# Kernel optimization log

Hardware: AMD Instinct MI355X
Metric: run time of the kernel (lower is better)

## Reference

```python
import jax, jax.numpy as jnp
import numpy as np

BASE_RES = 16; DESIRED_RES = 8192; LEVEL_INTERVAL = 2
LEVEL_DIM = 4; LOG2_HASH = 21
NUM_LEVELS = int(np.log(DESIRED_RES / BASE_RES) / np.log(LEVEL_INTERVAL)) + 1  # 10
MAX_PARAMS = 2 ** LOG2_HASH

def _level_metas():
    s = np.exp2(np.log2(DESIRED_RES / BASE_RES) / (NUM_LEVELS - 1))  # per-level scale = 2
    metas, off = [], 0
    for l in range(NUM_LEVELS):
        scale = BASE_RES * s ** l - 1.0
        res = int(np.ceil(scale)) + 1
        dense = res ** 3 <= MAX_PARAMS
        size = res ** 3 if dense else MAX_PARAMS
        size = int(np.ceil(size / 8) * 8)
        metas.append((scale, res, size, off, dense))
        off += size
    return metas, off

METAS, TABLE_SIZE = _level_metas()  # TABLE_SIZE = 14979072
OUT_DIM = NUM_LEVELS * LEVEL_DIM    # 40
PRIMES = (np.uint32(1), np.uint32(2654435761), np.uint32(805459861))

def contract(x):
    n = jnp.sqrt(jnp.maximum(jnp.sum(x * x, -1, keepdims=True), 1e-12))
    return jnp.where(n <= 1.0, x, (2.0 - 1.0 / n) * (x / n))

def grid_encode(x, table):
    # x: [N,3] in [0,1]; table: [TABLE_SIZE, LEVEL_DIM]. Multi-res hash grid, trilinear, align_corners=False.
    feats = []
    for scale, res, size, off, dense in METAS:
        pos = x * scale + 0.5
        p0f = jnp.floor(pos)
        f = pos - p0f  # trilinear fractions [N,3]
        p0 = p0f.astype(jnp.uint32)
        lvl = table[off:off + size]
        out = jnp.zeros((x.shape[0], LEVEL_DIM), x.dtype)
        for dx in (0, 1):
            for dy in (0, 1):
                for dz in (0, 1):
                    cx = p0[:, 0] + np.uint32(dx)
                    cy = p0[:, 1] + np.uint32(dy)
                    cz = p0[:, 2] + np.uint32(dz)
                    w = ((f[:, 0] if dx else 1.0 - f[:, 0]) *
                         (f[:, 1] if dy else 1.0 - f[:, 1]) *
                         (f[:, 2] if dz else 1.0 - f[:, 2]))
                    if dense:
                        idx = (cx * np.uint32(res) + cy) * np.uint32(res) + cz
                    else:
                        idx = (cx * PRIMES[0]) ^ (cy * PRIMES[1]) ^ (cz * PRIMES[2])
                    idx = (idx % np.uint32(size)).astype(jnp.int32)
                    out = out + w[:, None] * lvl[idx]
        feats.append(out)
    return jnp.concatenate(feats, -1)

def dir_enc(d):
    # pos_enc min_deg=0, max_deg=4, with_identity -> 3 + 2*3*4 = 27 dims
    scales = (2.0 ** jnp.arange(4)).astype(d.dtype)
    xb = (d[..., None, :] * scales[:, None]).reshape(d.shape[:-1] + (12,))
    return jnp.concatenate([d, jnp.sin(jnp.concatenate([xb, xb + 0.5 * jnp.pi], -1))], -1)

def _forward(coords, viewdirs, table, Wd0, bd0, Wd1, bd1, W0, b0, W1, b1, Wr, br):
    c = contract(coords) / 2.0          # warp_fn='contract', bound=2
    x01 = (c + 1.0) * 0.5               # encoder normalizes [-1,1] -> [0,1]
    N = int(np.prod(coords.shape[:-1]))
    feats = grid_encode(x01.reshape(N, 3), table).reshape(coords.shape[:-1] + (OUT_DIM,))
    h = jax.nn.relu(feats @ Wd0 + bd0)
    x = h @ Wd1 + bd1                   # bottleneck [..., 256]
    density = jax.nn.softplus(x[..., 0] - 1.0)  # density_bias = -1
    de = dir_enc(viewdirs)
    de = jnp.broadcast_to(de[..., None, :], x.shape[:-1] + (de.shape[-1],))
    inp = jnp.concatenate([x, de], -1)  # [..., 283]
    h = jax.nn.relu(inp @ W0 + b0)
    h = jnp.concatenate([h, inp], -1)   # skip at layer 0 -> [..., 539]
    h = jax.nn.relu(h @ W1 + b1)
    rgb = jax.nn.sigmoid(h @ Wr + br)   # premultiplier=1, rgb_bias=0
    rgb = rgb * (1.0 + 2 * 0.001) - 0.001  # rgb_padding
    return jnp.concatenate([density[..., None], rgb], -1)  # [..., 4]


def setup_inputs() -> dict:
    key = jax.random.key(0)
    ks = jax.random.split(key, 8)
    B, S = 4096, 32
    coords = jax.random.normal(ks[0], (B, S, 3), jnp.float32) * 1.5
    vd = jax.random.normal(ks[1], (B, 3), jnp.float32)
    viewdirs = vd / jnp.linalg.norm(vd, axis=-1, keepdims=True)
    table = jax.random.uniform(ks[2], (TABLE_SIZE, LEVEL_DIM), jnp.float32, -1e-4, 1e-4)
    def lin(k, i, o):
        s = 1.0 / np.sqrt(i)
        return jax.random.uniform(k, (i, o), jnp.float32, -s, s)
    BW, DE, NW = 256, 27, 256
    return dict(coords=coords, viewdirs=viewdirs, table=table,
                Wd0=lin(ks[3], OUT_DIM, 64), bd0=jnp.zeros((64,), jnp.float32),
                Wd1=lin(ks[4], 64, BW), bd1=jnp.zeros((BW,), jnp.float32),
                W0=lin(ks[5], BW + DE, NW), b0=jnp.zeros((NW,), jnp.float32),
                W1=lin(ks[6], NW + BW + DE, NW), b1=jnp.zeros((NW,), jnp.float32),
                Wr=lin(ks[7], NW, 3), br=jnp.zeros((3,), jnp.float32))


def reference(coords, viewdirs, table, Wd0, bd0, Wd1, bd1, W0, b0, W1, b1, Wr, br):
    return _forward(coords, viewdirs, table, Wd0, bd0, Wd1, bd1, W0, b0, W1, b1, Wr, br)
```

## Files before the change

### kernel.cpp

```cpp
#include <hip/hip_runtime.h>
#include <hip/hip_bf16.h>

#define NPTS (4096 * 32)

typedef __bf16 bf16x8 __attribute__((ext_vector_type(8)));
typedef float f32x4 __attribute__((ext_vector_type(4)));

__device__ __forceinline__ float bf2f(unsigned short u) {
    union { unsigned u32; float f; } v;
    v.u32 = ((unsigned)u) << 16;
    return v.f;
}
__device__ __forceinline__ unsigned short f2bf(float f) {
    __hip_bfloat16 h = __float2bfloat16(f);
    union { __hip_bfloat16 h; unsigned short u; } v;
    v.h = h;
    return v.u;
}

__global__ __launch_bounds__(256) void k_encode(const float* __restrict__ coords,
                                                const float* __restrict__ table,
                                                unsigned short* __restrict__ featsb) {
    int id = blockIdx.x * 256 + threadIdx.x;
    int n = id >> 1, p = id & 1;
    float x = coords[(size_t)n*3+0], y = coords[(size_t)n*3+1], z = coords[(size_t)n*3+2];
    float sq = x*x + y*y + z*z;
    float nn = sqrtf(fmaxf(sq, 1e-12f));
    if (nn > 1.0f) {
        float inv = 1.0f / nn;
        float s = 2.0f - inv;
        x = s * (x * inv); y = s * (y * inv); z = s * (z * inv);
    }
    float px = (x * 0.5f + 1.0f) * 0.5f;
    float py = (y * 0.5f + 1.0f) * 0.5f;
    float pz = (z * 0.5f + 1.0f) * 0.5f;
    const float4* tab = (const float4*)table;
    unsigned short* fr = featsb + (size_t)n * 64;
    constexpr unsigned OFFS[10] = {0u,4096u,36864u,299008u,2396160u,4493312u,6590464u,8687616u,10784768u,12881920u};
#pragma unroll
    for (int j = 0; j < 5; ++j) {
        int l2 = 2 * j;
        unsigned res   = p ? (16u << (l2+1)) : (16u << l2);
        float sc       = (float)(res - 1u);
        unsigned mask  = (l2+1 < 4 || !p) && (l2 < 4)
                         ? ((p ? (1u << (12+3*(l2+1))) : (1u << (12+3*l2))) - 1u)
                         : 2097151u;
        unsigned off   = p ? OFFS[l2+1] : OFFS[l2];
        bool dense     = (p ? (l2+1) : l2) < 4;
        const float4* tl = tab + off;
        float fx = px*sc + 0.5f, fy = py*sc + 0.5f, fz = pz*sc + 0.5f;
        float x0 = floorf(fx), y0 = floorf(fy), z0 = floorf(fz);
        float tx = fx - x0, ty = fy - y0, tz = fz - z0;
        unsigned cx = (unsigned)x0, cy = (unsigned)y0, cz = (unsigned)z0;
        float ax = 0.f, ay = 0.f, az = 0.f, aw = 0.f;
#pragma unroll
        for (int dx = 0; dx < 2; ++dx)
#pragma unroll
        for (int dy = 0; dy < 2; ++dy)
#pragma unroll
        for (int dz = 0; dz < 2; ++dz) {
            unsigned ux = cx + dx, uy = cy + dy, uz = cz + dz;
            unsigned idx;
            if (dense) idx = ((ux * res + uy) * res + uz) & mask;
            else       idx = (ux ^ (uy * 2654435761u) ^ (uz * 805459861u)) & mask;
            float w = (dx ? tx : 1.0f - tx) * (dy ? ty : 1.0f - ty) * (dz ? tz : 1.0f - tz);
            float4 v = tl[idx];
            ax += w * v.x; ay += w * v.y; az += w * v.z; aw += w * v.w;
        }
        ushort4 s;
        s.x = f2bf(ax); s.y = f2bf(ay); s.z = f2bf(az); s.w = f2bf(aw);
        *(ushort4*)(fr + (l2 + p) * 4) = s;
    }
    ushort4 z4; z4.x = z4.y = z4.z = z4.w = 0;
#pragma unroll
    for (int k = 40 + p * 4; k < 64; k += 8) *(ushort4*)(fr + k) = z4;
}

__global__ __launch_bounds__(256) void k_prep(const float* __restrict__ W0,
                                              const float* __restrict__ W1,
                                              const float* __restrict__ Wd0,
                                              const float* __restrict__ Wd1,
                                              unsigned short* __restrict__ W0t,
                                              unsigned short* __restrict__ W1t,
                                              unsigned short* __restrict__ Wd0t,
                                              unsigned short* __restrict__ Wd1t) {
    int i = blockIdx.x * 256 + threadIdx.x;
    if (i < 65536) {
        int c = i >> 8, k = i & 255;
        W0t[i] = f2bf(W0[(size_t)k * 256 + c]);
    }
    {
        int c = i >> 9, k = i & 511;
        W1t[i] = f2bf(W1[(size_t)k * 256 + c]);
    }
    if (i < 4608) {
        int c = i / 72, k = i % 72;
        Wd0t[i] = (k < 40) ? f2bf(Wd0[(size_t)k * 64 + c]) : 0;
    }
    if (i < 18432) {
        int c = i / 72, k = i % 72;
        Wd1t[i] = (k < 64) ? f2bf(Wd1[(size_t)k * 256 + c]) : 0;
    }
}

__global__ __launch_bounds__(256) void k_dirw(const float* __restrict__ vd,
                                              const float* __restrict__ W0,
                                              const float* __restrict__ b0,
                                              const float* __restrict__ W1,
                                              const float* __restrict__ b1,
                                              float* __restrict__ deW0,
                                              float* __restrict__ deW1) {
    __shared__ float de[27];
    int b = blockIdx.x;
    int t = threadIdx.x;
    if (t < 27) {
        float v;
        const float HPI = 0.5f * 3.14159265358979323846f;
        if (t < 3) {
            v = vd[(size_t)b*3 + t];
        } else if (t < 15) {
            int i = (t - 3) / 3, j = (t - 3) % 3;
            v = sinf(vd[(size_t)b*3 + j] * (float)(1 << i));
        } else {
            int i = (t - 15) / 3, j = (t - 15) % 3;
            v = sinf(vd[(size_t)b*3 + j] * (float)(1 << i) + HPI);
        }
        de[t] = v;
    }
    __syncthreads();
    float a0 = b0[t], a1 = b1[t];
#pragma unroll
    for (int k = 0; k < 27; ++k) {
        float d = de[k];
        a0 += d * W0[(size_t)(256 + k) * 256 + t];
        a1 += d * W1[(size_t)(512 + k) * 256 + t];
    }
    deW0[(size_t)b*256 + t] = a0;
    deW1[(size_t)b*256 + t] = a1;
}

__global__ __launch_bounds__(512, 4) void k_mlp0(const unsigned short* __restrict__ featsb,
                                                 const unsigned short* __restrict__ Wd0t,
                                                 const unsigned short* __restrict__ Wd1t,
                                                 const float* __restrict__ bd0,
                                                 const float* __restrict__ bd1,
                                                 unsigned short* __restrict__ xb,
                                                 float* __restrict__ out) {
    __shared__ __align__(16) unsigned short sWd1[256 * 72];
    __shared__ __align__(16) unsigned short sWd0[64 * 72];
    __shared__ __align__(16) unsigned short sF[64 * 72];
    __shared__ __align__(16) unsigned short sH[64 * 72];
    int t = threadIdx.x;
    int r0 = blockIdx.x * 64;
    {
        int r = t >> 3, kq = (t & 7) * 8;
        *(int4*)(sF + r * 72 + kq)   = *(const int4*)(featsb + (size_t)(r0 + r) * 64 + kq);
        *(int4*)(sWd0 + r * 72 + kq) = *(const int4*)(Wd0t + r * 72 + kq);
#pragma unroll
        for (int j = 0; j < 4; ++j) {
            int idx = t + j * 512;
            int c = idx >> 3, k = (idx & 7) * 8;
            *(int4*)(sWd1 + c * 72 + k) = *(const int4*)(Wd1t + c * 72 + k);
        }
    }
    __syncthreads();
    int lane = t & 63, wid = t >> 6, cl = lane & 15, q = lane >> 4;
    {
        int wr = wid >> 1, wc = wid & 1;
        f32x4 acc[2] = {};
#pragma unroll
        for (int ks = 0; ks < 2; ++ks) {
            bf16x8 af = *(const bf16x8*)(sF + (wr * 16 + cl) * 72 + ks * 32 + q * 8);
#pragma unroll
            for (int n = 0; n < 2; ++n) {
                bf16x8 bf = *(const bf16x8*)(sWd0 + (wc * 32 + n * 16 + cl) * 72 + ks * 32 + q * 8);
                acc[n] = __builtin_amdgcn_mfma_f32_16x16x32_bf16(af, bf, acc[n], 0, 0, 0);
            }
        }
#pragma unroll
        for (int n = 0; n < 2; ++n) {
            int c = wc * 32 + n * 16 + cl;
            float bv = bd0[c];
#pragma unroll
            for (int i = 0; i < 4; ++i) {
                int r = wr * 16 + q * 4 + i;
                sH[r * 72 + c] = f2bf(fmaxf(acc[n][i] + bv, 0.f));
            }
        }
    }
    __syncthreads();
    {
        int wr = wid >> 2, wc = wid & 3;
        f32x4 acc[2][4] = {};
#pragma unroll
        for (int ks = 0; ks < 2; ++ks) {
            bf16x8 af[2], bf[4];
#pragma unroll
            for (int m = 0; m < 2; ++m)
                af[m] = *(const bf16x8*)(sH + (wr * 32 + m * 16 + cl) * 72 + ks * 32 + q * 8);
#pragma unroll
            for (int n = 0; n < 4; ++n)
                bf[n] = *(const bf16x8*)(sWd1 + (wc * 64 + n * 16 + cl) * 72 + ks * 32 + q * 8);
#pragma unroll
            for (int m = 0; m < 2; ++m)
#pragma unroll
                for (int n = 0; n < 4; ++n)
                    acc[m][n] = __builtin_amdgcn_mfma_f32_16x16x32_bf16(af[m], bf[n], acc[m][n], 0, 0, 0);
        }
#pragma unroll
        for (int n = 0; n < 4; ++n) {
            int c = wc * 64 + n * 16 + cl;
            float bv = bd1[c];
#pragma unroll
            for (int m = 0; m < 2; ++m) {
#pragma unroll
                for (int i = 0; i < 4; ++i) {
                    int r = wr * 32 + m * 16 + q * 4 + i;
                    float v = acc[m][n][i] + bv;
                    xb[(size_t)(r0 + r) * 256 + c] = f2bf(v);
                    if (n == 0 && wc == 0 && cl == 0) {
                        float d = v - 1.0f;
                        float sp = fmaxf(d, 0.0f) + log1pf(expf(-fabsf(d)));
                        out[(size_t)(r0 + r) * 4] = sp;
                    }
                }
            }
        }
    }
}

__global__ __launch_bounds__(512, 2) void k_g34(const unsigned short* __restrict__ xb,
                                                const unsigned short* __restrict__ W0t,
                                                const unsigned short* __restrict__ W1t,
                                                const float* __restrict__ deW0,
                                                const float* __restrict__ deW1,
                                                const float* __restrict__ Wr,
                                                const float* __restrict__ br,
                                                float* __restrict__ out) {
    __shared__ __align__(16) unsigned short sH0[4][64 * 72];
    __shared__ __align__(16) unsigned short sB[256 * 40];
    __shared__ float sWr[768];
    int t = threadIdx.x;
    int lane = t & 63, wid = t >> 6;
    int wr = wid >> 2, wc = wid & 3;
    int cl = lane & 15, q = lane >> 4;
    int r0 = blockIdx.x * 64;
    for (int i = t; i < 768; i += 512) sWr[i] = Wr[i];

    int bc = t >> 1, bh = (t & 1) * 16;
    const unsigned short* W0p = W0t + (size_t)bc * 256 + bh;
    const unsigned short* W1p = W1t + (size_t)bc * 512 + bh;
    const unsigned short* Arow0 = xb + (size_t)(r0 + wr * 32 + cl) * 256 + q * 8;
    const unsigned short* Arow1 = Arow0 + 16 * 256;

    f32x4 acc1[2][4] = {};
    f32x4 acc2[2][4] = {};

    for (int c8 = 0; c8 < 8; ++c8) {
        int k0 = c8 * 32;
        bf16x8 af[2];
        af[0] = *(const bf16x8*)(Arow0 + k0);
        af[1] = *(const bf16x8*)(Arow1 + k0);
        int4 b0 = *(const int4*)(W0p + k0);
        int4 b1 = *(const int4*)(W0p + k0 + 8);
        __syncthreads();
        *(int4*)(sB + bc * 40 + bh)     = b0;
        *(int4*)(sB + bc * 40 + bh + 8) = b1;
        __syncthreads();
        {
            bf16x8 bf[4];
#pragma unroll
            for (int n = 0; n < 4; ++n)
                bf[n] = *(const bf16x8*)(sB + (wc * 64 + n * 16 + cl) * 40 + q * 8);
#pragma unroll
            for (int m = 0; m < 2; ++m)
#pragma unroll
                for (int n = 0; n < 4; ++n)
                    acc1[m][n] = __builtin_amdgcn_mfma_f32_16x16x32_bf16(af[m], bf[n], acc1[m][n], 0, 0, 0);
        }
        int4 c0 = *(const int4*)(W1p + 256 + k0);
        int4 c1 = *(const int4*)(W1p + 256 + k0 + 8);
        __syncthreads();
        *(int4*)(sB + bc * 40 + bh)     = c0;
        *(int4*)(sB + bc * 40 + bh + 8) = c1;
        __syncthreads();
        {
            bf16x8 bf[4];
#pragma unroll
            for (int n = 0; n < 4; ++n)
                bf[n] = *(const bf16x8*)(sB + (wc * 64 + n * 16 + cl) * 40 + q * 8);
#pragma unroll
            for (int m = 0; m < 2; ++m)
#pragma unroll
                for (int n = 0; n < 4; ++n)
                    acc2[m][n] = __builtin_amdgcn_mfma_f32_16x16x32_bf16(af[m], bf[n], acc2[m][n], 0, 0, 0);
        }
    }
#pragma unroll
    for (int m = 0; m < 2; ++m) {
        int rb = wr * 32 + m * 16;
        const float* dwp = deW0 + (size_t)((r0 + rb) >> 5) * 256;
#pragma unroll
        for (int n = 0; n < 4; ++n) {
            int c = wc * 64 + n * 16 + cl;
            float dv = dwp[c];
#pragma unroll
            for (int i = 0; i < 4; ++i) {
                int r = rb + q * 4 + i;
                sH0[wc][r * 72 + (c & 63)] = f2bf(fmaxf(acc1[m][n][i] + dv, 0.f));
            }
        }
    }
    __syncthreads();
    for (int c8 = 0; c8 < 8; ++c8) {
        int k0 = c8 * 32;
        bf16x8 af[2];
#pragma unroll
        for (int m = 0; m < 2; ++m)
            af[m] = *(const bf16x8*)(&sH0[k0 >> 6][(wr * 32 + m * 16 + cl) * 72 + (k0 & 63) + q * 8]);
        int4 b0 = *(const int4*)(W1p + k0);
        int4 b1 = *(const int4*)(W1p + k0 + 8);
        __syncthreads();
        *(int4*)(sB + bc * 40 + bh)     = b0;
        *(int4*)(sB + bc * 40 + bh + 8) = b1;
        __syncthreads();
        bf16x8 bf[4];
#pragma unroll
        for (int n = 0; n < 4; ++n)
            bf[n] = *(const bf16x8*)(sB + (wc * 64 + n * 16 + cl) * 40 + q * 8);
#pragma unroll
        for (int m = 0; m < 2; ++m)
#pragma unroll
            for (int n = 0; n < 4; ++n)
                acc2[m][n] = __builtin_amdgcn_mfma_f32_16x16x32_bf16(af[m], bf[n], acc2[m][n], 0, 0, 0);
    }
    __syncthreads();
    unsigned short* sH1 = &sH0[0][0];
#pragma unroll
    for (int m = 0; m < 2; ++m) {
        int rb = wr * 32 + m * 16;
        const float* dwp = deW1 + (size_t)((r0 + rb) >> 5) * 256;
#pragma unroll
        for (int n = 0; n < 4; ++n) {
            int c = wc * 64 + n * 16 + cl;
            float dv = dwp[c];
#pragma unroll
            for (int i = 0; i < 4; ++i) {
                int r = rb + q * 4 + i;
                sH1[r * 264 + c] = f2bf(fmaxf(acc2[m][n][i] + dv, 0.f));
            }
        }
    }
    __syncthreads();
    if (t < 384) {
        int r = t / 6, rem = t % 6, j = rem >> 1, half = rem & 1;
        float a = 0.f;
        const unsigned short* hp = sH1 + r * 264 + half * 128;
        const float* wp = sWr + (half * 128) * 3 + j;
        for (int c = 0; c < 128; ++c) a += bf2f(hp[c]) * wp[c * 3];
        a += __shfl_xor(a, 1);
        if (!half) {
            a += br[j];
            float s = 1.0f / (1.0f + expf(-a));
            out[(size_t)(r0 + r) * 4 + 1 + j] = s * 1.002f - 0.001f;
        }
    }
}

extern "C" void kernel_launch(void* const* d_in, const int* in_sizes, int n_in,
                              void* d_out, int out_size, void* d_ws, size_t ws_size,
                              hipStream_t stream) {
    const float* coords   = (const float*)d_in[0];
    const float* viewdirs = (const float*)d_in[1];
    const float* table    = (const float*)d_in[2];
    const float* Wd0      = (const float*)d_in[3];
    const float* bd0      = (const float*)d_in[4];
    const float* Wd1      = (const float*)d_in[5];
    const float* bd1      = (const float*)d_in[6];
    const float* W0       = (const float*)d_in[7];
    const float* b0       = (const float*)d_in[8];
    const float* W1       = (const float*)d_in[9];
    const float* b1       = (const float*)d_in[10];
    const float* Wr       = (const float*)d_in[11];
    const float* br       = (const float*)d_in[12];
    float* out = (float*)d_out;

    const size_t N = NPTS;
    unsigned short* ws = (unsigned short*)d_ws;
    unsigned short* featsb = ws;
    unsigned short* xb     = featsb + N * 64;
    float* deW0 = (float*)(xb + N * 256);
    float* deW1 = deW0 + 4096 * 256;
    unsigned short* W0t  = (unsigned short*)(deW1 + 4096 * 256);
    unsigned short* W1t  = W0t + 65536;
    unsigned short* Wd0t = W1t + 131072;
    unsigned short* Wd1t = Wd0t + 4608;

    k_encode<<<NPTS / 128, 256, 0, stream>>>(coords, table, featsb);
    k_prep<<<512, 256, 0, stream>>>(W0, W1, Wd0, Wd1, W0t, W1t, Wd0t, Wd1t);
    k_dirw<<<4096, 256, 0, stream>>>(viewdirs, W0, b0, W1, b1, deW0, deW1);
    k_mlp0<<<NPTS / 64, 512, 0, stream>>>(featsb, Wd0t, Wd1t, bd0, bd1, xb, out);
    k_g34<<<NPTS / 64, 512, 0, stream>>>(xb, W0t, W1t, deW0, deW1, Wr, br, out);
}
```

Measured before the change: 278.6 us.

## Batch hash-grid gathers per thread and restage g34 GEMM with register-prefetched B tiles

The encoder now gives each point to one thread. That thread handles two levels per iteration, issuing all 16 table gathers before accumulating, and writes 8 bf16 features in one 16-byte store. The aim is more memory-level parallelism and fewer stores. The k_g34 kernel stages the whole A tile in shared memory once and puts the two B operands in separate buffers, which halves the barriers in the first loop. It also prefetches the next B slice into registers and raises launch bounds to 4 blocks per CU. Risks are higher register pressure from forcing occupancy and fewer threads for encode latency hiding.

```diff
diff --git a/kernel.cpp b/kernel.cpp
--- a/kernel.cpp
+++ b/kernel.cpp
@@ -18,11 +18,37 @@
     return v.u;
 }
 
-__global__ __launch_bounds__(256) void k_encode(const float* __restrict__ coords,
+__device__ __forceinline__ void level_setup(int l, float px, float py, float pz,
+                                            unsigned idx[8], float w[8]) {
+    unsigned res = 16u << l;
+    float sc = (float)(res - 1u);
+    unsigned size = (l < 4) ? (res * res * res) : 2097152u;
+    unsigned mask = size - 1u;
+    float fx = px * sc + 0.5f, fy = py * sc + 0.5f, fz = pz * sc + 0.5f;
+    float x0 = floorf(fx), y0 = floorf(fy), z0 = floorf(fz);
+    float tx = fx - x0, ty = fy - y0, tz = fz - z0;
+    unsigned cx = (unsigned)x0, cy = (unsigned)y0, cz = (unsigned)z0;
+    int c = 0;
+#pragma unroll
+    for (int dx = 0; dx < 2; ++dx)
+#pragma unroll
+    for (int dy = 0; dy < 2; ++dy)
+#pragma unroll
+    for (int dz = 0; dz < 2; ++dz) {
+        unsigned ux = cx + dx, uy = cy + dy, uz = cz + dz;
+        unsigned id;
+        if (l < 4) id = ((ux * res + uy) * res + uz) & mask;
+        else       id = (ux ^ (uy * 2654435761u) ^ (uz * 805459861u)) & mask;
+        idx[c] = id;
+        w[c] = (dx ? tx : 1.0f - tx) * (dy ? ty : 1.0f - ty) * (dz ? tz : 1.0f - tz);
+        ++c;
+    }
+}
+
+__global__ __launch_bounds__(128) void k_encode(const float* __restrict__ coords,
                                                 const float* __restrict__ table,
                                                 unsigned short* __restrict__ featsb) {
-    int id = blockIdx.x * 256 + threadIdx.x;
-    int n = id >> 1, p = id & 1;
+    int n = blockIdx.x * 128 + threadIdx.x;
     float x = coords[(size_t)n*3+0], y = coords[(size_t)n*3+1], z = coords[(size_t)n*3+2];
     float sq = x*x + y*y + z*z;
     float nn = sqrtf(fmaxf(sq, 1e-12f));
@@ -38,42 +64,40 @@
     unsigned short* fr = featsb + (size_t)n * 64;
     constexpr unsigned OFFS[10] = {0u,4096u,36864u,299008u,2396160u,4493312u,6590464u,8687616u,10784768u,12881920u};
 #pragma unroll
-    for (int j = 0; j < 5; ++j) {
-        int l2 = 2 * j;
-        unsigned res   = p ? (16u << (l2+1)) : (16u << l2);
-        float sc       = (float)(res - 1u);
-        unsigned mask  = (l2+1 < 4 || !p) && (l2 < 4)
-                         ? ((p ? (1u << (12+3*(l2+1))) : (1u << (12+3*l2))) - 1u)
-                         : 2097151u;
-        unsigned off   = p ? OFFS[l2+1] : OFFS[l2];
-        bool dense     = (p ? (l2+1) : l2) < 4;
-        const float4* tl = tab + off;
-        float fx = px*sc + 0.5f, fy = py*sc + 0.5f, fz = pz*sc + 0.5f;
-        float x0 = floorf(fx), y0 = floorf(fy), z0 = floorf(fz);
-        float tx = fx - x0, ty = fy - y0, tz = fz - z0;
-        unsigned cx = (unsigned)x0, cy = (unsigned)y0, cz = (unsigned)z0;
+    for (int lp = 0; lp < 5; ++lp) {
+        const int lA = 2 * lp, lB = lA + 1;
+        unsigned iA[8], iB[8];
+        float wA[8], wB[8];
+        level_setup(lA, px, py, pz, iA, wA);
+        level_setup(lB, px, py, pz, iB, wB);
+        const float4* tA = tab + OFFS[lA];
+        const float4* tB = tab + OFFS[lB];
+        float4 vA[8], vB[8];
+#pragma unroll
+        for (int c = 0; c < 8; ++c) vA[c] = tA[iA[c]];
+#pragma unroll
+        for (int c = 0; c < 8; ++c) vB[c] = tB[iB[c]];
         float ax = 0.f, ay = 0.f, az = 0.f, aw = 0.f;
-#pragma unroll
-        for (int dx = 0; dx < 2; ++dx)
-#pragma unroll
-        for (int dy = 0; dy < 2; ++dy)
-#pragma unroll
-        for (int dz = 0; dz < 2; ++dz) {
-            unsigned ux = cx + dx, uy = cy + dy, uz = cz + dz;
-            unsigned idx;
-            if (dense) idx = ((ux * res + uy) * res + uz) & mask;
-            else       idx = (ux ^ (uy * 2654435761u) ^ (uz * 805459861u)) & mask;
-            float w = (dx ? tx : 1.0f - tx) * (dy ? ty : 1.0f - ty) * (dz ? tz : 1.0f - tz);
-            float4 v = tl[idx];
-            ax += w * v.x; ay += w * v.y; az += w * v.z; aw += w * v.w;
-        }
-        ushort4 s;
-        s.x = f2bf(ax); s.y = f2bf(ay); s.z = f2bf(az); s.w = f2bf(aw);
-        *(ushort4*)(fr + (l2 + p) * 4) = s;
-    }
-    ushort4 z4; z4.x = z4.y = z4.z = z4.w = 0;
-#pragma unroll
-    for (int k = 40 + p * 4; k < 64; k += 8) *(ushort4*)(fr + k) = z4;
+        float bx = 0.f, by = 0.f, bz = 0.f, bw = 0.f;
+#pragma unroll
+        for (int c = 0; c < 8; ++c) {
+            ax += wA[c] * vA[c].x; ay += wA[c] * vA[c].y;
+            az += wA[c] * vA[c].z; aw += wA[c] * vA[c].w;
+        }
+#pragma unroll
+        for (int c = 0; c < 8; ++c) {
+            bx += wB[c] * vB[c].x; by += wB[c] * vB[c].y;
+            bz += wB[c] * vB[c].z; bw += wB[c] * vB[c].w;
+        }
+        union { int4 q; unsigned short s[8]; } o;
+        o.s[0] = f2bf(ax); o.s[1] = f2bf(ay); o.s[2] = f2bf(az); o.s[3] = f2bf(aw);
+        o.s[4] = f2bf(bx); o.s[5] = f2bf(by); o.s[6] = f2bf(bz); o.s[7] = f2bf(bw);
+        *(int4*)(fr + lA * 4) = o.q;
+    }
+    int4 z4; z4.x = z4.y = z4.z = z4.w = 0;
+    *(int4*)(fr + 40) = z4;
+    *(int4*)(fr + 48) = z4;
+    *(int4*)(fr + 56) = z4;
 }
 
 __global__ __launch_bounds__(256) void k_prep(const float* __restrict__ W0,
@@ -229,7 +253,7 @@
     }
 }
 
-__global__ __launch_bounds__(512, 2) void k_g34(const unsigned short* __restrict__ xb,
+__global__ __launch_bounds__(512, 4) void k_g34(const unsigned short* __restrict__ xb,
                                                 const unsigned short* __restrict__ W0t,
                                                 const unsigned short* __restrict__ W1t,
                                                 const float* __restrict__ deW0,
@@ -237,9 +261,11 @@
                                                 const float* __restrict__ Wr,
                                                 const float* __restrict__ br,
                                                 float* __restrict__ out) {
-    __shared__ __align__(16) unsigned short sH0[4][64 * 72];
-    __shared__ __align__(16) unsigned short sB[256 * 40];
+    __shared__ __align__(16) unsigned short smem[38912];
     __shared__ float sWr[768];
+    unsigned short* sA  = smem;
+    unsigned short* sB0 = smem + 18432;
+    unsigned short* sB1 = smem + 28672;
     int t = threadIdx.x;
     int lane = t & 63, wid = t >> 6;
     int wr = wid >> 2, wc = wid & 3;
@@ -247,55 +273,65 @@
     int r0 = blockIdx.x * 64;
     for (int i = t; i < 768; i += 512) sWr[i] = Wr[i];
 
+    {
+        int r = t >> 3, ks = (t & 7) * 32;
+        const unsigned short* xr = xb + (size_t)(r0 + r) * 256 + ks;
+        int4 a0 = *(const int4*)(xr);
+        int4 a1 = *(const int4*)(xr + 8);
+        int4 a2 = *(const int4*)(xr + 16);
+        int4 a3 = *(const int4*)(xr + 24);
+        unsigned short* d = sA + (ks >> 6) * 4608 + r * 72 + (ks & 63);
+        *(int4*)(d)      = a0;
+        *(int4*)(d + 8)  = a1;
+        *(int4*)(d + 16) = a2;
+        *(int4*)(d + 24) = a3;
+    }
+
     int bc = t >> 1, bh = (t & 1) * 16;
-    const unsigned short* W0p = W0t + (size_t)bc * 256 + bh;
-    const unsigned short* W1p = W1t + (size_t)bc * 512 + bh;
-    const unsigned short* Arow0 = xb + (size_t)(r0 + wr * 32 + cl) * 256 + q * 8;
-    const unsigned short* Arow1 = Arow0 + 16 * 256;
+    const unsigned short* W0p  = W0t + (size_t)bc * 256 + bh;
+    const unsigned short* W1ph = W1t + (size_t)bc * 512 + 256 + bh;
+    const unsigned short* W1pl = W1t + (size_t)bc * 512 + bh;
 
     f32x4 acc1[2][4] = {};
     f32x4 acc2[2][4] = {};
 
+    int4 w0a = *(const int4*)(W0p);
+    int4 w0b = *(const int4*)(W0p + 8);
+    int4 w1a = *(const int4*)(W1ph);
+    int4 w1b = *(const int4*)(W1ph + 8);
     for (int c8 = 0; c8 < 8; ++c8) {
+        *(int4*)(sB0 + bc * 40 + bh)     = w0a;
+        *(int4*)(sB0 + bc * 40 + bh + 8) = w0b;
+        *(int4*)(sB1 + bc * 40 + bh)     = w1a;
+        *(int4*)(sB1 + bc * 40 + bh + 8) = w1b;
+        if (c8 < 7) {
+            int k1 = (c8 + 1) * 32;
+            w0a = *(const int4*)(W0p + k1);
+            w0b = *(const int4*)(W0p + k1 + 8);
+            w1a = *(const int4*)(W1ph + k1);
+            w1b = *(const int4*)(W1ph + k1 + 8);
+        }
+        __syncthreads();
         int k0 = c8 * 32;
-        bf16x8 af[2];
-        af[0] = *(const bf16x8*)(Arow0 + k0);
-        af[1] = *(const bf16x8*)(Arow1 + k0);
-        int4 b0 = *(const int4*)(W0p + k0);
-        int4 b1 = *(const int4*)(W0p + k0 + 8);
+        bf16x8 af[2], bf0[4], bf1[4];
+#pragma unroll
+        for (int m = 0; m < 2; ++m)
+            af[m] = *(const bf16x8*)(sA + (k0 >> 6) * 4608 + (wr * 32 + m * 16 + cl) * 72 + (k0 & 63) + q * 8);
+#pragma unroll
+        for (int n = 0; n < 4; ++n) {
+            bf0[n] = *(const bf16x8*)(sB0 + (wc * 64 + n * 16 + cl) * 40 + q * 8);
+            bf1[n] = *(const bf16x8*)(sB1 + (wc * 64 + n * 16 + cl) * 40 + q * 8);
+        }
+#pragma unroll
+        for (int m = 0; m < 2; ++m)
+#pragma unroll
+            for (int n = 0; n < 4; ++n) {
+                acc1[m][n] = __builtin_amdgcn_mfma_f32_16x16x32_bf16(af[m], bf0[n], acc1[m][n], 0, 0, 0);
+                acc2[m][n] = __builtin_amdgcn_mfma_f32_16x16x32_bf16(af[m], bf1[n], acc2[m][n], 0, 0, 0);
+            }
         __syncthreads();
-        *(int4*)(sB + bc * 40 + bh)     = b0;
-        *(int4*)(sB + bc * 40 + bh + 8) = b1;
-        __syncthreads();
-        {
-            bf16x8 bf[4];
-#pragma unroll
-            for (int n = 0; n < 4; ++n)
-                bf[n] = *(const bf16x8*)(sB + (wc * 64 + n * 16 + cl) * 40 + q * 8);
-#pragma unroll
-            for (int m = 0; m < 2; ++m)
-#pragma unroll
-                for (int n = 0; n < 4; ++n)
-                    acc1[m][n] = __builtin_amdgcn_mfma_f32_16x16x32_bf16(af[m], bf[n], acc1[m][n], 0, 0, 0);
-        }
-        int4 c0 = *(const int4*)(W1p + 256 + k0);
-        int4 c1 = *(const int4*)(W1p + 256 + k0 + 8);
-        __syncthreads();
-        *(int4*)(sB + bc * 40 + bh)     = c0;
-        *(int4*)(sB + bc * 40 + bh + 8) = c1;
-        __syncthreads();
-        {
-            bf16x8 bf[4];
-#pragma unroll
-            for (int n = 0; n < 4; ++n)
-                bf[n] = *(const bf16x8*)(sB + (wc * 64 + n * 16 + cl) * 40 + q * 8);
-#pragma unroll
-            for (int m = 0; m < 2; ++m)
-#pragma unroll
-                for (int n = 0; n < 4; ++n)
-                    acc2[m][n] = __builtin_amdgcn_mfma_f32_16x16x32_bf16(af[m], bf[n], acc2[m][n], 0, 0, 0);
-        }
-    }
+    }
+
 #pragma unroll
     for (int m = 0; m < 2; ++m) {
         int rb = wr * 32 + m * 16;
@@ -307,27 +343,32 @@
 #pragma unroll
             for (int i = 0; i < 4; ++i) {
                 int r = rb + q * 4 + i;
-                sH0[wc][r * 72 + (c & 63)] = f2bf(fmaxf(acc1[m][n][i] + dv, 0.f));
-            }
-        }
-    }
-    __syncthreads();
+                sA[wc * 4608 + r * 72 + (c & 63)] = f2bf(fmaxf(acc1[m][n][i] + dv, 0.f));
+            }
+        }
+    }
+    __syncthreads();
+
+    int4 v0 = *(const int4*)(W1pl);
+    int4 v1 = *(const int4*)(W1pl + 8);
     for (int c8 = 0; c8 < 8; ++c8) {
+        unsigned short* dst = (c8 & 1) ? sB1 : sB0;
+        *(int4*)(dst + bc * 40 + bh)     = v0;
+        *(int4*)(dst + bc * 40 + bh + 8) = v1;
+        if (c8 < 7) {
+            int k1 = (c8 + 1) * 32;
+            v0 = *(const int4*)(W1pl + k1);
+            v1 = *(const int4*)(W1pl + k1 + 8);
+        }
+        __syncthreads();
         int k0 = c8 * 32;
-        bf16x8 af[2];
+        bf16x8 af[2], bf[4];
 #pragma unroll
         for (int m = 0; m < 2; ++m)
-            af[m] = *(const bf16x8*)(&sH0[k0 >> 6][(wr * 32 + m * 16 + cl) * 72 + (k0 & 63) + q * 8]);
-        int4 b0 = *(const int4*)(W1p + k0);
-        int4 b1 = *(const int4*)(W1p + k0 + 8);
-        __syncthreads();
-        *(int4*)(sB + bc * 40 + bh)     = b0;
-        *(int4*)(sB + bc * 40 + bh + 8) = b1;
-        __syncthreads();
-        bf16x8 bf[4];
+            af[m] = *(const bf16x8*)(sA + (k0 >> 6) * 4608 + (wr * 32 + m * 16 + cl) * 72 + (k0 & 63) + q * 8);
 #pragma unroll
         for (int n = 0; n < 4; ++n)
-            bf[n] = *(const bf16x8*)(sB + (wc * 64 + n * 16 + cl) * 40 + q * 8);
+            bf[n] = *(const bf16x8*)(dst + (wc * 64 + n * 16 + cl) * 40 + q * 8);
 #pragma unroll
         for (int m = 0; m < 2; ++m)
 #pragma unroll
@@ -335,7 +376,8 @@
                 acc2[m][n] = __builtin_amdgcn_mfma_f32_16x16x32_bf16(af[m], bf[n], acc2[m][n], 0, 0, 0);
     }
     __syncthreads();
-    unsigned short* sH1 = &sH0[0][0];
+
+    unsigned short* sH1 = sA;
 #pragma unroll
     for (int m = 0; m < 2; ++m) {
         int rb = wr * 32 + m * 16;
@@ -396,7 +438,7 @@
     unsigned short* Wd0t = W1t + 131072;
     unsigned short* Wd1t = Wd0t + 4608;
 
-    k_encode<<<NPTS / 128, 256, 0, stream>>>(coords, table, featsb);
+    k_encode<<<NPTS / 128, 128, 0, stream>>>(coords, table, featsb);
     k_prep<<<512, 256, 0, stream>>>(W0, W1, Wd0, Wd1, W0t, W1t, Wd0t, Wd1t);
     k_dirw<<<4096, 256, 0, stream>>>(viewdirs, W0, b0, W1, b1, deW0, deW1);
     k_mlp0<<<NPTS / 64, 512, 0, stream>>>(featsb, Wd0t, Wd1t, bd0, bd1, xb, out);
```

Result: slower. 355.1 us (+27.5%).
